# Performance work log

Measured on AMD Instinct MI355X. Metric: run time of the kernel, lower is better.

Reference implementation:

```python
import jax, jax.numpy as jnp
import numpy as np

HEADS = 4


def rel_to_abs(x):
    """Convert relative logits [..., L, 2L-1] to absolute [..., L, L].
    out[..., i, j] = x[..., i, j - i + L - 1]."""
    L = x.shape[-2]
    idx = jnp.arange(L)[None, :] - jnp.arange(L)[:, None] + (L - 1)  # [L, L]
    idx = jnp.broadcast_to(idx, x.shape[:-1] + (L,))
    return jnp.take_along_axis(x, idx, axis=-1)


def setup_inputs() -> dict:
    key = jax.random.key(0)
    ks = jax.random.split(key, 5)
    b, c, h, w = 2, 256, 64, 64
    dh = c // HEADS
    return {
        "x": jax.random.normal(ks[0], (b, c, h, w), jnp.float32),
        "w_qkv": jax.random.normal(ks[1], (3 * c, c), jnp.float32) / np.float32(np.sqrt(c)),
        "w_out": jax.random.normal(ks[2], (c, c), jnp.float32) / np.float32(np.sqrt(c)),
        "rel_height": jax.random.normal(ks[3], (2 * h - 1, dh), jnp.float32),
        "rel_width": jax.random.normal(ks[4], (2 * w - 1, dh), jnp.float32),
    }


def reference(x, w_qkv, w_out, rel_height, rel_width):
    b, c, h, w = x.shape
    dh = c // HEADS
    N = h * w
    scale = dh ** -0.5

    # 1x1 conv == per-pixel matmul over channels
    qkv = jnp.einsum('bchw,oc->bohw', x, w_qkv)  # [b, 3c, h, w]
    q, k, v = jnp.split(qkv, 3, axis=1)

    def to_heads(t):  # [b, c, h, w] -> [b, H, N, dh]
        return t.reshape(b, HEADS, dh, N).transpose(0, 1, 3, 2)

    q = to_heads(q) * scale
    k = to_heads(k)
    v = to_heads(v)

    # content-content scores over spatial positions
    content = jnp.einsum('bnid,bnjd->bnij', q, k)  # [b, H, N, N]

    q5 = q.reshape(b, HEADS, h, w, dh)  # [b, H, x, y, dh]
    # width relative logits: [b,H,x,y,2w-1] -> abs -> [b,H,x,y,jw]
    rw = rel_to_abs(jnp.einsum('bnxyd,rd->bnxyr', q5, rel_width))
    # height relative logits on transposed spatial: [b,H,y,x,2h-1] -> [b,H,y,x,jh]
    rh = rel_to_abs(jnp.einsum('bnyxd,rd->bnyxr', q5.transpose(0, 1, 3, 2, 4), rel_height))

    logits = content.reshape(b, HEADS, h, w, h, w)
    logits = logits + rw[:, :, :, :, None, :]  # broadcast width bias over target height jh
    logits = logits + rh.transpose(0, 1, 3, 2, 4)[:, :, :, :, :, None]  # [b,H,x,y,jh] over jw

    attn = jax.nn.softmax(logits.reshape(b, HEADS, N, N), axis=-1)
    out = jnp.einsum('bnij,bnjd->bnid', attn, v)  # [b, H, N, dh]
    out = out.transpose(0, 1, 3, 2).reshape(b, c, h, w)
    out = jnp.einsum('bchw,oc->bohw', out, w_out)  # 1x1 out projection
    return out + x
```

## Files before the change

kernel.cpp:

```cpp
#include <hip/hip_runtime.h>

typedef unsigned short u16;
typedef unsigned int u32;
typedef __bf16 bf16x8 __attribute__((ext_vector_type(8)));
typedef __bf16 bf16x2 __attribute__((ext_vector_type(2)));
typedef float f32x4 __attribute__((ext_vector_type(4)));
typedef float f32x2 __attribute__((ext_vector_type(2)));
typedef u32 u32x4 __attribute__((ext_vector_type(4)));
typedef u32 u32x2 __attribute__((ext_vector_type(2)));

#define DEVI __device__ __forceinline__

#if defined(__has_builtin)
#if __has_builtin(__builtin_amdgcn_exp2f)
#define EXP2F(x) __builtin_amdgcn_exp2f(x)
#endif
#endif
#ifndef EXP2F
#define EXP2F(x) exp2f(x)
#endif

#define MFMA16(a, b, c) __builtin_amdgcn_mfma_f32_16x16x32_bf16(a, b, c, 0, 0, 0)

typedef __attribute__((address_space(1))) u32 gu32;
typedef __attribute__((address_space(3))) u32 lu32;
DEVI void gll16(const u16* g, u16* l) {
    __builtin_amdgcn_global_load_lds((const gu32*)g, (lu32*)l, 16, 0, 0);
}
#define WAIT_VM0() __builtin_amdgcn_s_waitcnt(0x0f70)

DEVI u16 f2bf(float f) {
    u32 u = __builtin_bit_cast(u32, f);
    u = (u + 0x7FFFu + ((u >> 16) & 1u)) >> 16;
    return (u16)u;
}
DEVI float bf2f(u16 h) {
    u32 u = ((u32)h) << 16;
    return __builtin_bit_cast(float, u);
}
DEVI float bfhi(u32 u) { return __builtin_bit_cast(float, u & 0xFFFF0000u); }
DEVI float bflo(u32 u) { return __builtin_bit_cast(float, u << 16); }
DEVI bf16x8 bc8(u32x4 u) { return __builtin_bit_cast(bf16x8, u); }
DEVI u32 pack2(float a, float b) {
    f32x2 v = {a, b};
    bf16x2 h = __builtin_convertvector(v, bf16x2);
    return __builtin_bit_cast(u32, h);
}

#define QSCALE 0.18033688011112042f

__global__ __launch_bounds__(256) void k_prep(const float* __restrict__ x,
                                              const float* __restrict__ wq,
                                              const float* __restrict__ wo,
                                              const float* __restrict__ relh,
                                              const float* __restrict__ relw,
                                              u16* __restrict__ xt, u16* __restrict__ wqb,
                                              u16* __restrict__ wob, u16* __restrict__ relhb,
                                              u16* __restrict__ relwb) {
    int bid = blockIdx.x;
    int t = threadIdx.x;
    if (bid < 512) {
        int pm = bid & 63, cm = (bid >> 6) & 3, b = bid >> 8;
        int p0 = pm * 64, c0 = cm * 64;
        __shared__ float tile[64][65];
#pragma unroll
        for (int it = 0; it < 4; ++it) {
            int idx = it * 256 + t;
            int cl = idx >> 4, f4 = idx & 15;
            f32x4 v = *(const f32x4*)(x + ((size_t)(b * 256 + c0 + cl)) * 4096 + p0 + f4 * 4);
            tile[cl][f4 * 4 + 0] = v[0];
            tile[cl][f4 * 4 + 1] = v[1];
            tile[cl][f4 * 4 + 2] = v[2];
            tile[cl][f4 * 4 + 3] = v[3];
        }
        __syncthreads();
#pragma unroll
        for (int it = 0; it < 2; ++it) {
            int idx = it * 256 + t;
            int pl = idx >> 3, g = idx & 7;
            u32x4 pk;
            pk.x = pack2(tile[g * 8 + 0][pl], tile[g * 8 + 1][pl]);
            pk.y = pack2(tile[g * 8 + 2][pl], tile[g * 8 + 3][pl]);
            pk.z = pack2(tile[g * 8 + 4][pl], tile[g * 8 + 5][pl]);
            pk.w = pack2(tile[g * 8 + 6][pl], tile[g * 8 + 7][pl]);
            *(u32x4*)(xt + ((size_t)(b * 4096 + p0 + pl)) * 256 + c0 + g * 8) = pk;
        }
    } else {
        int i0 = (bid - 512) * 256 + t;
#pragma unroll
        for (int i = i0; i < 196608; i += 65536) wqb[i] = f2bf(wq[i]);
        if (i0 < 65536) wob[i0] = f2bf(wo[i0]);
        if (i0 < 8192) {
            relhb[i0] = (i0 < 8128) ? f2bf(relh[i0]) : (u16)0;
            relwb[i0] = (i0 < 8128) ? f2bf(relw[i0]) : (u16)0;
        }
    }
}

__global__ __launch_bounds__(256) void k_qkv(const u16* __restrict__ xt, const u16* __restrict__ wqb,
                                             const u16* __restrict__ relwb,
                                             const u16* __restrict__ relhb,
                                             u16* __restrict__ q, u16* __restrict__ k,
                                             u16* __restrict__ vt, u16* __restrict__ Wabs,
                                             u16* __restrict__ HabsT) {
    int pm = blockIdx.x, on = blockIdx.y, b = blockIdx.z;
    int p0 = pm * 64, o0 = on * 64;
    __shared__ __align__(16) u16 Sm[64 * 256];
    int t = threadIdx.x;
    int wv = t >> 6, l = t & 63, quad = l >> 4, li = l & 15;

    u32x4 areg[8];
    const u32x4* arow = (const u32x4*)(xt + ((size_t)(b * 4096 + p0 + wv * 16 + li)) * 256);
#pragma unroll
    for (int kc = 0; kc < 8; ++kc) areg[kc] = arow[kc * 4 + quad];

    {
        int pc = l & 31;
#pragma unroll
        for (int i = 0; i < 8; ++i) {
            int r = wv * 16 + i * 2 + (l >> 5);
            gll16(wqb + (size_t)(o0 + r) * 256 + ((pc + r) & 31) * 8,
                  Sm + (wv * 16 + i * 2) * 256);
        }
    }
    WAIT_VM0();
    __syncthreads();

    f32x4 acc[4] = {{0, 0, 0, 0}, {0, 0, 0, 0}, {0, 0, 0, 0}, {0, 0, 0, 0}};
#pragma unroll
    for (int kc = 0; kc < 8; ++kc) {
        bf16x8 a = bc8(areg[kc]);
#pragma unroll
        for (int ct = 0; ct < 4; ++ct) {
            bf16x8 bb = bc8(*(const u32x4*)(Sm + (ct * 16 + li) * 256 +
                                            (((kc * 4 + quad) - (ct * 16 + li)) & 31) * 8));
            acc[ct] = MFMA16(a, bb, acc[ct]);
        }
    }

    int tensor = on >> 2, head = on & 3;
    if (tensor == 2) {
        __syncthreads();
        u16* T = Sm;
#pragma unroll
        for (int ct = 0; ct < 4; ++ct)
#pragma unroll
            for (int r = 0; r < 4; ++r)
                T[(ct * 16 + li) * 72 + wv * 16 + quad * 4 + r] = f2bf(acc[ct][r]);
        __syncthreads();
        int dr = t >> 2, pc = (t & 3) * 16;
        u32x4* g = (u32x4*)(vt + ((size_t)((b * 4 + head) * 64 + dr)) * 4096 + p0 + pc);
        const u32x4* s2 = (const u32x4*)(T + dr * 72 + pc);
        g[0] = s2[0];
        g[1] = s2[1];
    } else {
        u16* outp = (tensor == 0) ? q : k;
        float sc = (tensor == 0) ? QSCALE : 1.0f;
#pragma unroll
        for (int ct = 0; ct < 4; ++ct)
#pragma unroll
            for (int r = 0; r < 4; ++r) {
                int p = p0 + wv * 16 + quad * 4 + r;
                int d = ct * 16 + li;
                outp[((size_t)((b * 4 + head) * 4096 + p)) * 64 + d] = f2bf(acc[ct][r] * sc);
            }
        if (tensor == 0) {
            int bh = b * 4 + head;
            u16* T = Sm;
            u16* Ls = Sm + 64 * 72;
            __syncthreads();
#pragma unroll
            for (int ct = 0; ct < 4; ++ct)
#pragma unroll
                for (int r = 0; r < 4; ++r)
                    T[(wv * 16 + quad * 4 + r) * 72 + ct * 16 + li] = f2bf(acc[ct][r] * QSCALE);
            {
                int row = t >> 1, half = t & 1;
                const u32x4* g2 = (const u32x4*)(relwb + row * 64 + half * 32);
                u32x4* s2 = (u32x4*)(Ls + row * 72 + half * 32);
#pragma unroll
                for (int kk = 0; kk < 4; ++kk) s2[kk] = g2[kk];
            }
            __syncthreads();
            u32x4 aq2[2];
            aq2[0] = *(const u32x4*)(T + (wv * 16 + li) * 72 + quad * 8);
            aq2[1] = *(const u32x4*)(T + (wv * 16 + li) * 72 + 32 + quad * 8);

            f32x4 acc2[8];
#pragma unroll
            for (int ct = 0; ct < 8; ++ct) acc2[ct] = (f32x4){0.f, 0.f, 0.f, 0.f};
#pragma unroll
            for (int kc = 0; kc < 2; ++kc) {
                bf16x8 a = bc8(aq2[kc]);
#pragma unroll
                for (int ct = 0; ct < 8; ++ct) {
                    bf16x8 bb = bc8(*(const u32x4*)(Ls + (ct * 16 + li) * 72 + kc * 32 + quad * 8));
                    acc2[ct] = MFMA16(a, bb, acc2[ct]);
                }
            }
#pragma unroll
            for (int ct = 0; ct < 8; ++ct)
#pragma unroll
                for (int r = 0; r < 4; ++r) {
                    int row = wv * 16 + quad * 4 + r;
                    int j = (ct * 16 + li) - 63 + row;
                    if (j >= 0 && j < 64)
                        Wabs[((size_t)(bh * 4096 + p0 + row)) * 64 + j] = f2bf(acc2[ct][r]);
                }
            __syncthreads();
            {
                int row = t >> 1, half = t & 1;
                const u32x4* g2 = (const u32x4*)(relhb + row * 64 + half * 32);
                u32x4* s2 = (u32x4*)(Ls + row * 72 + half * 32);
#pragma unroll
                for (int kk = 0; kk < 4; ++kk) s2[kk] = g2[kk];
            }
            __syncthreads();
#pragma unroll
            for (int ct = 0; ct < 8; ++ct) acc2[ct] = (f32x4){0.f, 0.f, 0.f, 0.f};
#pragma unroll
            for (int kc = 0; kc < 2; ++kc) {
                bf16x8 a = bc8(aq2[kc]);
#pragma unroll
                for (int ct = 0; ct < 8; ++ct) {
                    bf16x8 bb = bc8(*(const u32x4*)(Ls + (ct * 16 + li) * 72 + kc * 32 + quad * 8));
                    acc2[ct] = MFMA16(a, bb, acc2[ct]);
                }
            }
#pragma unroll
            for (int ct = 0; ct < 8; ++ct)
#pragma unroll
                for (int r = 0; r < 4; ++r) {
                    int row = wv * 16 + quad * 4 + r;
                    int j = (ct * 16 + li) - 63 + pm;
                    if (j >= 0 && j < 64)
                        HabsT[((size_t)(bh * 64 + j)) * 4096 + p0 + row] = f2bf(acc2[ct][r]);
                }
        }
    }
}

__global__ __launch_bounds__(256, 2) void k_flash(const u16* __restrict__ q,
                                                  const u16* __restrict__ kg,
                                                  const u16* __restrict__ vt,
                                                  const u16* __restrict__ Wabs,
                                                  const u16* __restrict__ HabsT,
                                                  u16* __restrict__ OP,
                                                  float* __restrict__ LS) {
    int pm = blockIdx.x, bh = blockIdx.y, ks = blockIdx.z;
    int p0 = pm * 128;
    __shared__ __align__(16) u16 Kt[2][64 * 72];
    __shared__ __align__(16) u16 Vl[2][64 * 72];
    int t = threadIdx.x, wv = t >> 6, l = t & 63, quad = l >> 4, li = l & 15;
    int rbase = wv * 32;

    u32x4 aq[2][2];
#pragma unroll
    for (int rs = 0; rs < 2; ++rs) {
        const u32x4* qrow =
            (const u32x4*)(q + ((size_t)(bh * 4096 + p0 + rbase + rs * 16 + li)) * 64);
        aq[rs][0] = qrow[quad];
        aq[rs][1] = qrow[4 + quad];
    }

    f32x4 wb4[2][4];
#pragma unroll
    for (int rs = 0; rs < 2; ++rs)
#pragma unroll
        for (int ct = 0; ct < 4; ++ct) {
            int jcol = ((ct >> 1) * 32) + quad * 8 + ((ct & 1) * 4);
            const u32* wp = (const u32*)(Wabs +
                                         ((size_t)(bh * 4096 + p0 + rbase + rs * 16 + li)) * 64 +
                                         jcol);
            u32 lo = wp[0], hi = wp[1];
            wb4[rs][ct] = (f32x4){bflo(lo), bfhi(lo), bflo(hi), bfhi(hi)};
        }

    const u16* hbase = HabsT + ((size_t)(bh * 64 + ks * 16)) * 4096 + p0 + rbase;

    int srow = t >> 2, scc = (t & 3) * 16;
    int krow = ((srow >> 5) * 2 + ((srow >> 2) & 1)) * 16 + ((srow >> 3) & 3) * 4 + (srow & 3);
    {
        int j0 = ks * 1024;
        const u32x4* gk = (const u32x4*)(kg + ((size_t)(bh * 4096 + j0 + srow)) * 64 + scc);
        u32x4* sk = (u32x4*)(Kt[0] + krow * 72 + scc);
        sk[0] = gk[0];
        sk[1] = gk[1];
        const u32x4* gv = (const u32x4*)(vt + ((size_t)(bh * 64 + srow)) * 4096 + j0 + scc);
        u32x4* sv = (u32x4*)(Vl[0] + srow * 72 + scc);
        sv[0] = gv[0];
        sv[1] = gv[1];
    }
    u16 hc0 = hbase[li];
    u16 hc1 = hbase[16 + li];

    f32x4 oacc[2][5];
#pragma unroll
    for (int rs = 0; rs < 2; ++rs)
#pragma unroll
        for (int ct = 0; ct < 5; ++ct) oacc[rs][ct] = (f32x4){0.f, 0.f, 0.f, 0.f};

    const u32x4 ones = {0x3F803F80u, 0x3F803F80u, 0x3F803F80u, 0x3F803F80u};

    u32x4 kreg[2], vreg[2];
    u16 hn0, hn1;
    for (int kt = 0; kt < 16; ++kt) {
        __syncthreads();
        int cur = kt & 1;
        const u16* Kc = Kt[cur];
        const u16* Vc = Vl[cur];
        if (kt < 15) {
            int j0 = (ks * 16 + kt + 1) * 64;
            const u32x4* gk = (const u32x4*)(kg + ((size_t)(bh * 4096 + j0 + srow)) * 64 + scc);
            kreg[0] = gk[0];
            kreg[1] = gk[1];
            const u32x4* gv = (const u32x4*)(vt + ((size_t)(bh * 64 + srow)) * 4096 + j0 + scc);
            vreg[0] = gv[0];
            vreg[1] = gv[1];
            hn0 = hbase[(size_t)(kt + 1) * 4096 + li];
            hn1 = hbase[(size_t)(kt + 1) * 4096 + 16 + li];
        }

        float hh0 = bf2f(hc0);
        float hh1 = bf2f(hc1);
        f32x4 s[2][4];
#pragma unroll
        for (int ct = 0; ct < 4; ++ct) {
            s[0][ct] = wb4[0][ct] + hh0;
            s[1][ct] = wb4[1][ct] + hh1;
        }
#pragma unroll
        for (int kc = 0; kc < 2; ++kc) {
            bf16x8 b0 = bc8(aq[0][kc]), b1 = bc8(aq[1][kc]);
#pragma unroll
            for (int ct = 0; ct < 4; ++ct) {
                bf16x8 af = bc8(*(const u32x4*)(Kc + (ct * 16 + li) * 72 + kc * 32 + quad * 8));
                s[0][ct] = MFMA16(af, b0, s[0][ct]);
                s[1][ct] = MFMA16(af, b1, s[1][ct]);
            }
        }

        u32x4 pf[2][2];
#pragma unroll
        for (int rs = 0; rs < 2; ++rs)
#pragma unroll
            for (int p = 0; p < 2; ++p) {
                u32x4 pp;
                pp.x = pack2(EXP2F(s[rs][2 * p][0]), EXP2F(s[rs][2 * p][1]));
                pp.y = pack2(EXP2F(s[rs][2 * p][2]), EXP2F(s[rs][2 * p][3]));
                pp.z = pack2(EXP2F(s[rs][2 * p + 1][0]), EXP2F(s[rs][2 * p + 1][1]));
                pp.w = pack2(EXP2F(s[rs][2 * p + 1][2]), EXP2F(s[rs][2 * p + 1][3]));
                pf[rs][p] = pp;
            }

#pragma unroll
        for (int dt = 0; dt < 4; ++dt) {
            const u16* vr = Vc + (dt * 16 + li) * 72 + quad * 8;
            u32x4 B0 = *(const u32x4*)(vr);
            u32x4 B1 = *(const u32x4*)(vr + 32);
            oacc[0][dt] = MFMA16(bc8(pf[0][0]), bc8(B0), oacc[0][dt]);
            oacc[1][dt] = MFMA16(bc8(pf[1][0]), bc8(B0), oacc[1][dt]);
            oacc[0][dt] = MFMA16(bc8(pf[0][1]), bc8(B1), oacc[0][dt]);
            oacc[1][dt] = MFMA16(bc8(pf[1][1]), bc8(B1), oacc[1][dt]);
        }
#pragma unroll
        for (int p = 0; p < 2; ++p) {
            oacc[0][4] = MFMA16(bc8(pf[0][p]), bc8(ones), oacc[0][4]);
            oacc[1][4] = MFMA16(bc8(pf[1][p]), bc8(ones), oacc[1][4]);
        }

        if (kt < 15) {
            u32x4* sk = (u32x4*)(Kt[cur ^ 1] + krow * 72 + scc);
            sk[0] = kreg[0];
            sk[1] = kreg[1];
            u32x4* sv = (u32x4*)(Vl[cur ^ 1] + srow * 72 + scc);
            sv[0] = vreg[0];
            sv[1] = vreg[1];
            hc0 = hn0;
            hc1 = hn1;
        }
    }

#pragma unroll
    for (int rs = 0; rs < 2; ++rs) {
#pragma unroll
        for (int ct = 0; ct < 4; ++ct)
#pragma unroll
            for (int r = 0; r < 4; ++r) {
                int p = p0 + rbase + rs * 16 + quad * 4 + r;
                OP[((size_t)((ks * 8 + bh) * 4096 + p)) * 64 + ct * 16 + li] =
                    f2bf(oacc[rs][ct][r]);
            }
        if (li == 0) {
#pragma unroll
            for (int r = 0; r < 4; ++r) {
                int p = p0 + rbase + rs * 16 + quad * 4 + r;
                LS[(size_t)(ks * 8 + bh) * 4096 + p] = oacc[rs][4][r];
            }
        }
    }
}

__global__ __launch_bounds__(256) void k_out2(const u16* __restrict__ wob,
                                              const u16* __restrict__ OP,
                                              const float* __restrict__ LS,
                                              const float* __restrict__ x,
                                              float* __restrict__ out) {
    int pm = blockIdx.x, b = blockIdx.y, coh = blockIdx.z;
    int p0 = pm * 64;
    __shared__ __align__(16) u16 Bt[64 * 264];
    int t = threadIdx.x, wv = t >> 6, l = t & 63, quad = l >> 4, li = l & 15;

    {
        int row = t >> 2, head = t & 3;
        int bh = b * 4 + head;
        int p = p0 + row;
        const u32x4* o0p = (const u32x4*)(OP + ((size_t)(bh * 4096 + p)) * 64);
        const u32x4* o1p = (const u32x4*)(OP + ((size_t)((8 + bh) * 4096 + p)) * 64);
        const u32x4* o2p = (const u32x4*)(OP + ((size_t)((16 + bh) * 4096 + p)) * 64);
        const u32x4* o3p = (const u32x4*)(OP + ((size_t)((24 + bh) * 4096 + p)) * 64);
        float linv = 1.0f / (LS[(size_t)bh * 4096 + p] + LS[(size_t)(8 + bh) * 4096 + p] +
                             LS[(size_t)(16 + bh) * 4096 + p] + LS[(size_t)(24 + bh) * 4096 + p]);
        u16* dst = Bt + row * 264 + head * 64;
#pragma unroll
        for (int kk = 0; kk < 8; ++kk) {
            u32x4 a = o0p[kk], c = o1p[kk], d = o2p[kk], e = o3p[kk];
            u32x4 pk;
            pk.x = pack2((bflo(a.x) + bflo(c.x) + bflo(d.x) + bflo(e.x)) * linv,
                         (bfhi(a.x) + bfhi(c.x) + bfhi(d.x) + bfhi(e.x)) * linv);
            pk.y = pack2((bflo(a.y) + bflo(c.y) + bflo(d.y) + bflo(e.y)) * linv,
                         (bfhi(a.y) + bfhi(c.y) + bfhi(d.y) + bfhi(e.y)) * linv);
            pk.z = pack2((bflo(a.z) + bflo(c.z) + bflo(d.z) + bflo(e.z)) * linv,
                         (bfhi(a.z) + bfhi(c.z) + bfhi(d.z) + bfhi(e.z)) * linv);
            pk.w = pack2((bflo(a.w) + bflo(c.w) + bflo(d.w) + bflo(e.w)) * linv,
                         (bfhi(a.w) + bfhi(c.w) + bfhi(d.w) + bfhi(e.w)) * linv);
            *(u32x4*)(dst + kk * 8) = pk;
        }
    }
    __syncthreads();

#pragma unroll
    for (int ci = 0; ci < 2; ++ci) {
        int com = coh * 2 + ci;
        int co0 = com * 64;
        f32x4 acc[4] = {{0, 0, 0, 0}, {0, 0, 0, 0}, {0, 0, 0, 0}, {0, 0, 0, 0}};
        const u32x4* arow = (const u32x4*)(wob + (size_t)(co0 + wv * 16 + li) * 256);
#pragma unroll
        for (int kc = 0; kc < 8; ++kc) {
            bf16x8 a = bc8(arow[kc * 4 + quad]);
#pragma unroll
            for (int ct = 0; ct < 4; ++ct) {
                bf16x8 bb = bc8(*(const u32x4*)(Bt + (ct * 16 + li) * 264 + kc * 32 + quad * 8));
                acc[ct] = MFMA16(a, bb, acc[ct]);
            }
        }
#pragma unroll
        for (int ct = 0; ct < 4; ++ct)
#pragma unroll
            for (int r = 0; r < 4; ++r) {
                size_t idx =
                    ((size_t)(b * 256 + co0 + wv * 16 + quad * 4 + r)) * 4096 + p0 + ct * 16 + li;
                out[idx] = acc[ct][r] + x[idx];
            }
    }
}

extern "C" void kernel_launch(void* const* d_in, const int* in_sizes, int n_in, void* d_out,
                              int out_size, void* d_ws, size_t ws_size, hipStream_t stream) {
    const float* x = (const float*)d_in[0];
    const float* wqkv = (const float*)d_in[1];
    const float* wout = (const float*)d_in[2];
    const float* relh = (const float*)d_in[3];
    const float* relw = (const float*)d_in[4];
    float* out = (float*)d_out;
    char* ws = (char*)d_ws;

    u16* xt = (u16*)(ws + 0);
    u16* wqb = (u16*)(ws + 4194304);
    u16* wob = (u16*)(ws + 4587520);
    u16* relwb = (u16*)(ws + 4718592);
    u16* relhb = (u16*)(ws + 4734976);
    u16* qb = (u16*)(ws + 4751360);
    u16* kb = (u16*)(ws + 8945664);
    u16* vtb = (u16*)(ws + 13139968);
    u16* Wabs = (u16*)(ws + 17334272);
    u16* HabsT = (u16*)(ws + 21528576);
    u16* OPart = (u16*)(ws + 25722880);
    float* LSum = (float*)(ws + 0);

    k_prep<<<768, 256, 0, stream>>>(x, wqkv, wout, relh, relw, xt, wqb, wob, relhb, relwb);
    k_qkv<<<dim3(64, 12, 2), 256, 0, stream>>>(xt, wqb, relwb, relhb, qb, kb, vtb, Wabs, HabsT);
    k_flash<<<dim3(32, 8, 4), 256, 0, stream>>>(qb, kb, vtb, Wabs, HabsT, OPart, LSum);
    k_out2<<<dim3(64, 2, 2), 256, 0, stream>>>(wob, OPart, LSum, x, out);
}
```

Baseline: 145.6 us.

## Double flash query tile per wave and load K/V directly into swizzled LDS

Each block in the attention kernel now covers 256 query rows instead of 128, and each wave handles 64 rows, so every K/V tile staged in shared memory is reused by twice as many MFMAs. The grid is halved to match. K/V tiles are now copied from global memory straight into LDS with an XOR-swizzled unpadded layout, replacing the register round trip and the padded rows. The width bias is kept packed as bf16 in registers, and score computation is interleaved with exp per column tile. In exchange the kernel holds more registers, which may lower occupancy, and the smaller grid gives fewer blocks per CU.

```diff
diff --git a/kernel.cpp b/kernel.cpp
--- a/kernel.cpp
+++ b/kernel.cpp
@@ -248,141 +248,136 @@
                                                   u16* __restrict__ OP,
                                                   float* __restrict__ LS) {
     int pm = blockIdx.x, bh = blockIdx.y, ks = blockIdx.z;
-    int p0 = pm * 128;
-    __shared__ __align__(16) u16 Kt[2][64 * 72];
-    __shared__ __align__(16) u16 Vl[2][64 * 72];
+    int p0 = pm * 256;
+    __shared__ __align__(16) u16 Kt[2][64 * 64];
+    __shared__ __align__(16) u16 Vl[2][64 * 64];
     int t = threadIdx.x, wv = t >> 6, l = t & 63, quad = l >> 4, li = l & 15;
-    int rbase = wv * 32;
-
-    u32x4 aq[2][2];
-#pragma unroll
-    for (int rs = 0; rs < 2; ++rs) {
+    int rbase = wv * 64;
+
+    u32x4 aq[4][2];
+#pragma unroll
+    for (int rs = 0; rs < 4; ++rs) {
         const u32x4* qrow =
             (const u32x4*)(q + ((size_t)(bh * 4096 + p0 + rbase + rs * 16 + li)) * 64);
         aq[rs][0] = qrow[quad];
         aq[rs][1] = qrow[4 + quad];
     }
 
-    f32x4 wb4[2][4];
-#pragma unroll
-    for (int rs = 0; rs < 2; ++rs)
+    u32x2 wbp[4][4];
+#pragma unroll
+    for (int rs = 0; rs < 4; ++rs)
 #pragma unroll
         for (int ct = 0; ct < 4; ++ct) {
             int jcol = ((ct >> 1) * 32) + quad * 8 + ((ct & 1) * 4);
             const u32* wp = (const u32*)(Wabs +
                                          ((size_t)(bh * 4096 + p0 + rbase + rs * 16 + li)) * 64 +
                                          jcol);
-            u32 lo = wp[0], hi = wp[1];
-            wb4[rs][ct] = (f32x4){bflo(lo), bfhi(lo), bflo(hi), bfhi(hi)};
+            wbp[rs][ct] = (u32x2){wp[0], wp[1]};
         }
 
     const u16* hbase = HabsT + ((size_t)(bh * 64 + ks * 16)) * 4096 + p0 + rbase;
 
-    int srow = t >> 2, scc = (t & 3) * 16;
-    int krow = ((srow >> 5) * 2 + ((srow >> 2) & 1)) * 16 + ((srow >> 3) & 3) * 4 + (srow & 3);
-    {
-        int j0 = ks * 1024;
-        const u32x4* gk = (const u32x4*)(kg + ((size_t)(bh * 4096 + j0 + srow)) * 64 + scc);
-        u32x4* sk = (u32x4*)(Kt[0] + krow * 72 + scc);
-        sk[0] = gk[0];
-        sk[1] = gk[1];
-        const u32x4* gv = (const u32x4*)(vt + ((size_t)(bh * 64 + srow)) * 4096 + j0 + scc);
-        u32x4* sv = (u32x4*)(Vl[0] + srow * 72 + scc);
-        sv[0] = gv[0];
-        sv[1] = gv[1];
-    }
-    u16 hc0 = hbase[li];
-    u16 hc1 = hbase[16 + li];
-
-    f32x4 oacc[2][5];
-#pragma unroll
-    for (int rs = 0; rs < 2; ++rs)
+    int ln3 = l >> 3, ln7 = l & 7;
+    int xo = (ln7 ^ ln3) * 8;
+    int R0 = wv * 8 + ln3, R1 = 32 + R0;
+    int j0r = (R0 & 32) | ((R0 & 16) >> 2) | ((R0 & 8) << 1) | ((R0 & 4) << 1) | (R0 & 3);
+    int j1r = (R1 & 32) | ((R1 & 16) >> 2) | ((R1 & 8) << 1) | ((R1 & 4) << 1) | (R1 & 3);
+    const u16* kS0 = kg + ((size_t)(bh * 4096 + ks * 1024 + j0r)) * 64 + xo;
+    const u16* kS1 = kg + ((size_t)(bh * 4096 + ks * 1024 + j1r)) * 64 + xo;
+    const u16* vS0 = vt + ((size_t)(bh * 64 + R0)) * 4096 + ks * 1024 + xo;
+    const u16* vS1 = vt + ((size_t)(bh * 64 + R1)) * 4096 + ks * 1024 + xo;
+    int ldst = wv * 512;
+
+    int o0 = li * 64 + ((quad ^ ln7) * 8);
+    int o1 = li * 64 + (((quad + 4) ^ ln7) * 8);
+
+    gll16(kS0, Kt[0] + ldst);
+    gll16(kS1, Kt[0] + 2048 + ldst);
+    gll16(vS0, Vl[0] + ldst);
+    gll16(vS1, Vl[0] + 2048 + ldst);
+    u16 hc[4];
+#pragma unroll
+    for (int rs = 0; rs < 4; ++rs) hc[rs] = hbase[rs * 16 + li];
+    WAIT_VM0();
+
+    f32x4 oacc[4][5];
+#pragma unroll
+    for (int rs = 0; rs < 4; ++rs)
 #pragma unroll
         for (int ct = 0; ct < 5; ++ct) oacc[rs][ct] = (f32x4){0.f, 0.f, 0.f, 0.f};
 
     const u32x4 ones = {0x3F803F80u, 0x3F803F80u, 0x3F803F80u, 0x3F803F80u};
 
-    u32x4 kreg[2], vreg[2];
-    u16 hn0, hn1;
     for (int kt = 0; kt < 16; ++kt) {
         __syncthreads();
         int cur = kt & 1;
         const u16* Kc = Kt[cur];
         const u16* Vc = Vl[cur];
+        u16 hn[4];
         if (kt < 15) {
-            int j0 = (ks * 16 + kt + 1) * 64;
-            const u32x4* gk = (const u32x4*)(kg + ((size_t)(bh * 4096 + j0 + srow)) * 64 + scc);
-            kreg[0] = gk[0];
-            kreg[1] = gk[1];
-            const u32x4* gv = (const u32x4*)(vt + ((size_t)(bh * 64 + srow)) * 4096 + j0 + scc);
-            vreg[0] = gv[0];
-            vreg[1] = gv[1];
-            hn0 = hbase[(size_t)(kt + 1) * 4096 + li];
-            hn1 = hbase[(size_t)(kt + 1) * 4096 + 16 + li];
-        }
-
-        float hh0 = bf2f(hc0);
-        float hh1 = bf2f(hc1);
-        f32x4 s[2][4];
+            kS0 += 4096;
+            kS1 += 4096;
+            vS0 += 64;
+            vS1 += 64;
+            u16* Kn = Kt[cur ^ 1];
+            u16* Vn = Vl[cur ^ 1];
+            gll16(kS0, Kn + ldst);
+            gll16(kS1, Kn + 2048 + ldst);
+            gll16(vS0, Vn + ldst);
+            gll16(vS1, Vn + 2048 + ldst);
+#pragma unroll
+            for (int rs = 0; rs < 4; ++rs) hn[rs] = hbase[(size_t)(kt + 1) * 4096 + rs * 16 + li];
+        }
+
+        u32x4 pf[4][2];
 #pragma unroll
         for (int ct = 0; ct < 4; ++ct) {
-            s[0][ct] = wb4[0][ct] + hh0;
-            s[1][ct] = wb4[1][ct] + hh1;
-        }
-#pragma unroll
-        for (int kc = 0; kc < 2; ++kc) {
-            bf16x8 b0 = bc8(aq[0][kc]), b1 = bc8(aq[1][kc]);
-#pragma unroll
-            for (int ct = 0; ct < 4; ++ct) {
-                bf16x8 af = bc8(*(const u32x4*)(Kc + (ct * 16 + li) * 72 + kc * 32 + quad * 8));
-                s[0][ct] = MFMA16(af, b0, s[0][ct]);
-                s[1][ct] = MFMA16(af, b1, s[1][ct]);
-            }
-        }
-
-        u32x4 pf[2][2];
-#pragma unroll
-        for (int rs = 0; rs < 2; ++rs)
-#pragma unroll
-            for (int p = 0; p < 2; ++p) {
-                u32x4 pp;
-                pp.x = pack2(EXP2F(s[rs][2 * p][0]), EXP2F(s[rs][2 * p][1]));
-                pp.y = pack2(EXP2F(s[rs][2 * p][2]), EXP2F(s[rs][2 * p][3]));
-                pp.z = pack2(EXP2F(s[rs][2 * p + 1][0]), EXP2F(s[rs][2 * p + 1][1]));
-                pp.w = pack2(EXP2F(s[rs][2 * p + 1][2]), EXP2F(s[rs][2 * p + 1][3]));
-                pf[rs][p] = pp;
-            }
+            bf16x8 af0 = bc8(*(const u32x4*)(Kc + ct * 1024 + o0));
+            bf16x8 af1 = bc8(*(const u32x4*)(Kc + ct * 1024 + o1));
+#pragma unroll
+            for (int rs = 0; rs < 4; ++rs) {
+                float hh = bf2f(hc[rs]);
+                u32x2 w = wbp[rs][ct];
+                f32x4 s4 = {bflo(w.x) + hh, bfhi(w.x) + hh, bflo(w.y) + hh, bfhi(w.y) + hh};
+                s4 = MFMA16(af0, bc8(aq[rs][0]), s4);
+                s4 = MFMA16(af1, bc8(aq[rs][1]), s4);
+                u32 pa = pack2(EXP2F(s4[0]), EXP2F(s4[1]));
+                u32 pb = pack2(EXP2F(s4[2]), EXP2F(s4[3]));
+                if (ct & 1) {
+                    pf[rs][ct >> 1].z = pa;
+                    pf[rs][ct >> 1].w = pb;
+                } else {
+                    pf[rs][ct >> 1].x = pa;
+                    pf[rs][ct >> 1].y = pb;
+                }
+            }
+        }
 
 #pragma unroll
         for (int dt = 0; dt < 4; ++dt) {
-            const u16* vr = Vc + (dt * 16 + li) * 72 + quad * 8;
-            u32x4 B0 = *(const u32x4*)(vr);
-            u32x4 B1 = *(const u32x4*)(vr + 32);
-            oacc[0][dt] = MFMA16(bc8(pf[0][0]), bc8(B0), oacc[0][dt]);
-            oacc[1][dt] = MFMA16(bc8(pf[1][0]), bc8(B0), oacc[1][dt]);
-            oacc[0][dt] = MFMA16(bc8(pf[0][1]), bc8(B1), oacc[0][dt]);
-            oacc[1][dt] = MFMA16(bc8(pf[1][1]), bc8(B1), oacc[1][dt]);
-        }
-#pragma unroll
-        for (int p = 0; p < 2; ++p) {
-            oacc[0][4] = MFMA16(bc8(pf[0][p]), bc8(ones), oacc[0][4]);
-            oacc[1][4] = MFMA16(bc8(pf[1][p]), bc8(ones), oacc[1][4]);
+            bf16x8 B0 = bc8(*(const u32x4*)(Vc + dt * 1024 + o0));
+            bf16x8 B1 = bc8(*(const u32x4*)(Vc + dt * 1024 + o1));
+#pragma unroll
+            for (int rs = 0; rs < 4; ++rs) {
+                oacc[rs][dt] = MFMA16(bc8(pf[rs][0]), B0, oacc[rs][dt]);
+                oacc[rs][dt] = MFMA16(bc8(pf[rs][1]), B1, oacc[rs][dt]);
+            }
+        }
+#pragma unroll
+        for (int rs = 0; rs < 4; ++rs) {
+            oacc[rs][4] = MFMA16(bc8(pf[rs][0]), bc8(ones), oacc[rs][4]);
+            oacc[rs][4] = MFMA16(bc8(pf[rs][1]), bc8(ones), oacc[rs][4]);
         }
 
         if (kt < 15) {
-            u32x4* sk = (u32x4*)(Kt[cur ^ 1] + krow * 72 + scc);
-            sk[0] = kreg[0];
-            sk[1] = kreg[1];
-            u32x4* sv = (u32x4*)(Vl[cur ^ 1] + srow * 72 + scc);
-            sv[0] = vreg[0];
-            sv[1] = vreg[1];
-            hc0 = hn0;
-            hc1 = hn1;
-        }
-    }
-
-#pragma unroll
-    for (int rs = 0; rs < 2; ++rs) {
+            WAIT_VM0();
+#pragma unroll
+            for (int rs = 0; rs < 4; ++rs) hc[rs] = hn[rs];
+        }
+    }
+
+#pragma unroll
+    for (int rs = 0; rs < 4; ++rs) {
 #pragma unroll
         for (int ct = 0; ct < 4; ++ct)
 #pragma unroll
@@ -490,6 +485,6 @@
 
     k_prep<<<768, 256, 0, stream>>>(x, wqkv, wout, relh, relw, xt, wqb, wob, relhb, relwb);
     k_qkv<<<dim3(64, 12, 2), 256, 0, stream>>>(xt, wqb, relwb, relhb, qb, kb, vtb, Wabs, HabsT);
-    k_flash<<<dim3(32, 8, 4), 256, 0, stream>>>(qb, kb, vtb, Wabs, HabsT, OPart, LSum);
+    k_flash<<<dim3(16, 8, 4), 256, 0, stream>>>(qb, kb, vtb, Wabs, HabsT, OPart, LSum);
     k_out2<<<dim3(64, 2, 2), 256, 0, stream>>>(wob, OPart, LSum, x, out);
 }
```

Result: no change. 144.9 us (-0.5%).
